# Kernel optimization log

Hardware: AMD Instinct MI355X
Metric: run time of the kernel (lower is better)

Reference implementation:

```python
import jax, jax.numpy as jnp
import numpy as np
import math

N, E, C, A, M, B, H = 50000, 600000, 32, 32, 32, 10, 64


def setup_inputs() -> dict:
    key = jax.random.key(0)
    ks = jax.random.split(key, 14)
    f = jnp.float32
    node_input = jax.random.normal(ks[0], (N, C), f)
    node_attr = jax.random.normal(ks[1], (N, A), f)
    node_deg = 1.0 + 31.0 * jax.random.uniform(ks[2], (N, 1), dtype=f)  # degrees >= 1
    edge_src = jax.random.randint(ks[3], (E,), 0, N, jnp.int32)
    edge_dst = jax.random.randint(ks[4], (E,), 0, N, jnp.int32)
    edge_attr = jax.random.normal(ks[5], (E, 9), f)  # SH up to lmax=2: 1+3+5
    edge_length_embedded = jax.random.uniform(ks[6], (E, B), dtype=f)
    w_lin_in = jax.random.normal(ks[7], (C, A, C), f)    # FCTP(Cx0e, Ax0e -> Cx0e)
    w_lin_mask = jax.random.normal(ks[8], (C, A, M), f)  # FCTP scalar block of linear_mask
    w_out0 = jax.random.normal(ks[9], (C, A, M), f)      # linear_output, l=0 block
    w_out1 = jax.random.normal(ks[10], (C, A, M), f)     # l=1 block
    w_out2 = jax.random.normal(ks[11], (C, A, M), f)     # l=2 block
    W0 = jax.random.normal(ks[12], (B, H), f)            # radial net (edge2weight)
    W1 = jax.random.normal(ks[13], (H, 3 * C), f)        # -> tensor_edge.weight_numel = 3C ('uvu', v=1)
    return dict(node_input=node_input, node_attr=node_attr, node_deg=node_deg,
                edge_src=edge_src, edge_dst=edge_dst, edge_attr=edge_attr,
                edge_length_embedded=edge_length_embedded,
                w_lin_in=w_lin_in, w_lin_mask=w_lin_mask,
                w_out0=w_out0, w_out1=w_out1, w_out2=w_out2, W0=W0, W1=W1,
                numb=100, n=8)


def reference(node_input, node_attr, node_deg, edge_src, edge_dst, edge_attr,
              edge_length_embedded, w_lin_in, w_lin_mask, w_out0, w_out1, w_out2,
              W0, W1, numb, n):
    # GraphConvolution.forward with irreps_in=Cx0e, irreps_node_attr=Ax0e,
    # irreps_edge_attr=1x0e+1x1o+1x2e (lmax=2), irreps_out=Mx0e+Mx1o+Mx2e.
    nN = node_input.shape[0]
    inv_ca = 1.0 / math.sqrt(C * A)

    def fctp_scalar(x, z, w):  # FullyConnectedTensorProduct with all-scalar in1/in2
        return jnp.einsum('nu,nv,uvk->nk', x, z, w) * inv_ca

    # linear_input, then node_deg normalization
    h0 = fctp_scalar(node_input, node_attr, w_lin_in)            # [N, C]
    deg_isqrt = 1.0 / jnp.sqrt(node_deg)                          # [N, 1]
    nf = h0 * deg_isqrt
    # linear_mask: only 0e outputs have tp paths (scalars x scalars); 1o/2e are zero
    mask_scalar = fctp_scalar(node_input, node_attr, w_lin_mask)  # [N, M]

    # edge2weight radial MLP (e3nn FullyConnectedNet style: /sqrt(fan_in), silu hidden)
    h = jax.nn.silu(edge_length_embedded @ W0 * (1.0 / math.sqrt(B)))
    ew = h @ W1 * (1.0 / math.sqrt(H))                            # [E, 3C]
    w0e, w1o, w2e = ew[:, :C], ew[:, C:2 * C], ew[:, 2 * C:]

    # tensor_edge: 'uvu' 0e(x)l->l paths: out[u,m] = w[u]*x_src[u]*Y_l[m]
    xs = nf[edge_src]                                             # gather [E, C]
    m0 = (w0e * xs) * edge_attr[:, :1]                            # [E, C]
    m1 = (w1o * xs)[:, :, None] * edge_attr[:, None, 1:4]         # [E, C, 3]
    m2 = (w2e * xs)[:, :, None] * edge_attr[:, None, 4:9]         # [E, C, 5]

    # scatter-reduce to destination nodes, then deg normalization
    a0 = jax.ops.segment_sum(m0, edge_dst, num_segments=nN) * deg_isqrt
    a1 = jax.ops.segment_sum(m1, edge_dst, num_segments=nN) * deg_isqrt[:, :, None]
    a2 = jax.ops.segment_sum(m2, edge_dst, num_segments=nN) * deg_isqrt[:, :, None]

    # linear_output: FCTP(mid, Ax0e -> out); scalar attr mixes multiplicities per l
    out0 = jnp.einsum('nu,nv,uvk->nk', a0, node_attr, w_out0) * inv_ca        # [N, M]
    out1 = jnp.einsum('num,nv,uvk->nkm', a1, node_attr, w_out1) * inv_ca      # [N, M, 3]
    out2 = jnp.einsum('num,nv,uvk->nkm', a2, node_attr, w_out2) * inv_ca      # [N, M, 5]

    # c_s * node_mask + c_x * node_output; output_mask is 1 on 0e, 0 on 1o/2e
    c_s, c_x = math.sin(math.pi / 8), math.cos(math.pi / 8)
    scal = c_s * mask_scalar + c_x * out0
    return jnp.concatenate([scal, out1.reshape(nN, 3 * M), out2.reshape(nN, 5 * M)], axis=1)
```

## Files before the change

### kernel.cpp

```cpp
#include <hip/hip_runtime.h>

#define NC 32
#define NA 32
#define NB 10
#define NH 64

typedef __attribute__((ext_vector_type(8))) short bf16x8;
typedef __attribute__((ext_vector_type(4))) float f32x4;

static __device__ __forceinline__ unsigned short f2bf(float f) {
  union { float f; unsigned u; } v; v.f = f;
  unsigned r = v.u + 0x7fffu + ((v.u >> 16) & 1u);
  return (unsigned short)(r >> 16);
}
static __device__ __forceinline__ float bf2f(unsigned short b) {
  union { unsigned u; float f; } v; v.u = ((unsigned)b) << 16;
  return v.f;
}

__global__ void k_prep(const float* __restrict__ nattr, const float* __restrict__ ndeg,
                       const float* __restrict__ w0, const float* __restrict__ w1,
                       const float* __restrict__ w2, const float* __restrict__ w3,
                       const float* __restrict__ w4, const float* __restrict__ W1g,
                       unsigned short* __restrict__ zb, float* __restrict__ dis,
                       unsigned short* __restrict__ wrp, unsigned short* __restrict__ w1p,
                       int N) {
  int i = blockIdx.x * 256 + threadIdx.x;
  int nz = N * NC;
  if (i < nz) { zb[i] = f2bf(nattr[i]); return; }
  i -= nz;
  if (i < N) { dis[i] = rsqrtf(ndeg[i]); return; }
  i -= N;
  if (i < 5 * 32768) {
    int T = i >> 15, r = i & 32767;
    int t = r >> 9, l = (r >> 3) & 63, b = r & 7;
    int j = t * 16 + (l & 15);
    int u = j >> 5, k = j & 31, v = 8 * (l >> 4) + b;
    const float* w = (T == 0) ? w0 : (T == 1) ? w1 : (T == 2) ? w2 : (T == 3) ? w3 : w4;
    wrp[T * 32768 + (t * 64 + l) * 8 + b] = f2bf(w[u * 1024 + v * 32 + k] * (1.0f / 32.0f));
    return;
  }
  i -= 5 * 32768;
  if (i < 6144) {
    int c = i / 3072, r2 = i % 3072;
    int t = r2 >> 9, l = (r2 >> 3) & 63, b = r2 & 7;
    int k = 32 * c + 8 * (l >> 4) + b, col = 16 * t + (l & 15);
    w1p[i] = f2bf(W1g[k * 96 + col] * 0.125f);
  }
}

__global__ __launch_bounds__(512) void k_fctp(
    const unsigned short* __restrict__ wrp, const unsigned short* __restrict__ zb,
    const float* __restrict__ xp, int nm, int xnstr, int xoff,
    float* __restrict__ outp, int onstr,
    const float* __restrict__ scalep,
    const float* __restrict__ addp, float selfc, float addc) {
  __shared__ float zw[16 * 1025];
  __shared__ float xl[16][5][32];
  int tid = threadIdx.x;
  int lane = tid & 63, wv = tid >> 6;
  int nbase = blockIdx.x << 4;

  for (int i = tid; i < 16 * nm * 32; i += 512) {
    int n = i / (nm * 32); int rem = i - n * (nm * 32); int m = rem >> 5, u = rem & 31;
    xl[n][m][u] = xp[(nbase + n) * xnstr + xoff + m * 32 + u];
  }

  bf16x8 af = *(const bf16x8*)(zb + (nbase + (lane & 15)) * 32 + 8 * (lane >> 4));
  f32x4 acc[8];
#pragma unroll
  for (int i2 = 0; i2 < 8; ++i2) {
    int t = wv * 8 + i2;
    bf16x8 bfr = *(const bf16x8*)(wrp + (t * 64 + lane) * 8);
    f32x4 z4 = {0.f, 0.f, 0.f, 0.f};
    acc[i2] = __builtin_amdgcn_mfma_f32_16x16x32_bf16(af, bfr, z4, 0, 0, 0);
  }
  int rb = 4 * (lane >> 4);
#pragma unroll
  for (int i2 = 0; i2 < 8; ++i2) {
    int col = (wv * 8 + i2) * 16 + (lane & 15);
#pragma unroll
    for (int r = 0; r < 4; ++r) zw[(rb + r) * 1025 + col] = acc[i2][r];
  }
  __syncthreads();

  int n = tid >> 5, k = tid & 31;
  float sc = scalep ? scalep[nbase + n] : 1.0f;
  const float* zr = &zw[n * 1025];
  for (int m = 0; m < nm; ++m) {
    float s = 0.f;
#pragma unroll
    for (int u = 0; u < 32; ++u) s = fmaf(xl[n][m][u], zr[u * 32 + k], s);
    s *= sc;
    if (addp) s = selfc * s + addc * addp[(nbase + n) * 32 + k];
    outp[(nbase + n) * onstr + k * nm + m] = s;
  }
}

__global__ void k_count(const int* __restrict__ dst, int* __restrict__ cnt, int E) {
  int i = blockIdx.x * 256 + threadIdx.x;
  if (i < E) atomicAdd(&cnt[dst[i]], 1);
}
__global__ __launch_bounds__(512) void k_scan1(const int* __restrict__ cnt, int* __restrict__ exl,
                                               int* __restrict__ bsum, int n) {
  __shared__ int s[512];
  int t = threadIdx.x;
  int i = blockIdx.x * 512 + t;
  int v = (i < n) ? cnt[i] : 0;
  s[t] = v;
  __syncthreads();
  for (int off = 1; off < 512; off <<= 1) {
    int add = (t >= off) ? s[t - off] : 0;
    __syncthreads();
    s[t] += add;
    __syncthreads();
  }
  if (i < n) exl[i] = s[t] - v;
  if (t == 511) bsum[blockIdx.x] = s[511];
}
__global__ void k_scan2(int* __restrict__ bsum, int nb) {
  __shared__ int s[128];
  int t = threadIdx.x;
  int v = (t < nb) ? bsum[t] : 0;
  s[t] = v;
  __syncthreads();
  for (int off = 1; off < 128; off <<= 1) {
    int add = (t >= off) ? s[t - off] : 0;
    __syncthreads();
    s[t] += add;
    __syncthreads();
  }
  if (t < nb) bsum[t] = s[t] - v;
}
__global__ void k_scan3(int* __restrict__ off, const int* __restrict__ bbase,
                        int* __restrict__ cur, int N, int E) {
  int i = blockIdx.x * 256 + threadIdx.x;
  if (i < N) {
    int o = off[i] + bbase[i >> 9];
    off[i] = o;
    cur[i] = o;
  } else if (i == N) {
    off[N] = E;
  }
}
__global__ void k_fill(const int* __restrict__ dst, int* __restrict__ cur,
                       int* __restrict__ pos, int E) {
  int i = blockIdx.x * 256 + threadIdx.x;
  if (i < E) {
    pos[i] = atomicAdd(&cur[dst[i]], 1);
  }
}

__global__ __launch_bounds__(256) void k_mlp(const float* __restrict__ el,
                                             const float* __restrict__ W0g,
                                             const unsigned short* __restrict__ w1p,
                                             const int* __restrict__ pos,
                                             const int* __restrict__ esrc,
                                             const float* __restrict__ eattr,
                                             unsigned short* __restrict__ ewP,
                                             int* __restrict__ esrcP,
                                             float* __restrict__ eattrP, int E) {
  __shared__ float w0s[NB * NH];
  __shared__ __align__(16) unsigned short tile[64 * 104];
  __shared__ int posl[64];
  int tid = threadIdx.x;
  int ebase = blockIdx.x * 64;
  for (int i = tid; i < NB * NH; i += 256) w0s[i] = W0g[i] * 0.31622776601683794f;
  if (tid < 64) posl[tid] = pos[ebase + tid];
  __syncthreads();

  for (int i = tid; i < 64 * 10; i += 256) {
    int le = i / 10, c = i - le * 10;
    int p = posl[le];
    int e = ebase + le;
    if (c == 0) esrcP[p] = esrc[e];
    else eattrP[(size_t)p * 9 + (c - 1)] = eattr[(size_t)e * 9 + (c - 1)];
  }

  int lane = tid & 63, wv = tid >> 6;
  int eloc0 = wv * 16;
  int erow = ebase + eloc0 + (lane & 15);
  float elr[NB];
#pragma unroll
  for (int b = 0; b < NB; ++b) elr[b] = el[erow * NB + b];
  int g8 = 8 * (lane >> 4);
  bf16x8 afr[2];
#pragma unroll
  for (int c = 0; c < 2; ++c) {
#pragma unroll
    for (int b = 0; b < 8; ++b) {
      int j = 32 * c + g8 + b;
      float p = 0.f;
#pragma unroll
      for (int q = 0; q < NB; ++q) p = fmaf(elr[q], w0s[q * NH + j], p);
      float h = p / (1.f + __expf(-p));
      afr[c][b] = (short)f2bf(h);
    }
  }
  f32x4 acc[6];
#pragma unroll
  for (int t = 0; t < 6; ++t) { f32x4 z4 = {0.f, 0.f, 0.f, 0.f}; acc[t] = z4; }
#pragma unroll
  for (int c = 0; c < 2; ++c) {
#pragma unroll
    for (int t = 0; t < 6; ++t) {
      bf16x8 bfr = *(const bf16x8*)(w1p + ((c * 6 + t) * 64 + lane) * 8);
      acc[t] = __builtin_amdgcn_mfma_f32_16x16x32_bf16(afr[c], bfr, acc[t], 0, 0, 0);
    }
  }
  int rb = 4 * (lane >> 4);
#pragma unroll
  for (int t = 0; t < 6; ++t) {
    int col = 16 * t + (lane & 15);
#pragma unroll
    for (int r = 0; r < 4; ++r) {
      tile[(eloc0 + rb + r) * 104 + col] = f2bf(acc[t][r]);
    }
  }
  __syncthreads();
  for (int ch = tid; ch < 64 * 12; ch += 256) {
    int le = ch / 12, seg = ch - le * 12;
    int p = posl[le];
    *(uint4*)(ewP + (size_t)p * 96 + seg * 8) =
        *(const uint4*)(&tile[le * 104 + seg * 8]);
  }
}

__global__ __launch_bounds__(256) void k_gather(
    const int* __restrict__ off, const int* __restrict__ esrcP,
    const float* __restrict__ eattrP, const unsigned short* __restrict__ ewP,
    const float* __restrict__ nf, const float* __restrict__ dis,
    float* __restrict__ a_all, int N) {
  int hw = (blockIdx.x * 256 + threadIdx.x) >> 5;
  int u = threadIdx.x & 31;
  if (hw >= N) return;
  int beg = off[hw], end = off[hw + 1];
  float a0 = 0, a1x = 0, a1y = 0, a1z = 0, b0 = 0, b1 = 0, b2 = 0, b3 = 0, b4 = 0;
  float xs_next = 0.f;
  if (beg < end) {
    int s0 = esrcP[beg];
    xs_next = nf[(size_t)s0 * 32 + u];
  }
  for (int p = beg; p < end; ++p) {
    float xs = xs_next;
    if (p + 1 < end) {
      int s2 = esrcP[p + 1];
      xs_next = nf[(size_t)s2 * 32 + u];
    }
    const unsigned short* ewr = ewP + (size_t)p * 96;
    float w0 = bf2f(ewr[u]), w1 = bf2f(ewr[32 + u]), w2 = bf2f(ewr[64 + u]);
    const float* ea = eattrP + (size_t)p * 9;
    float t0 = w0 * xs, t1 = w1 * xs, t2 = w2 * xs;
    a0  = fmaf(t0, ea[0], a0);
    a1x = fmaf(t1, ea[1], a1x);
    a1y = fmaf(t1, ea[2], a1y);
    a1z = fmaf(t1, ea[3], a1z);
    b0  = fmaf(t2, ea[4], b0);
    b1  = fmaf(t2, ea[5], b1);
    b2  = fmaf(t2, ea[6], b2);
    b3  = fmaf(t2, ea[7], b3);
    b4  = fmaf(t2, ea[8], b4);
  }
  float d = dis[hw];
  float* ar = a_all + (size_t)hw * 288;
  ar[0 * 32 + u] = a0 * d;
  ar[1 * 32 + u] = a1x * d;
  ar[2 * 32 + u] = a1y * d;
  ar[3 * 32 + u] = a1z * d;
  ar[4 * 32 + u] = b0 * d;
  ar[5 * 32 + u] = b1 * d;
  ar[6 * 32 + u] = b2 * d;
  ar[7 * 32 + u] = b3 * d;
  ar[8 * 32 + u] = b4 * d;
}

extern "C" void kernel_launch(void* const* d_in, const int* in_sizes, int n_in,
                              void* d_out, int out_size, void* d_ws, size_t ws_size,
                              hipStream_t stream) {
  const float* node_input = (const float*)d_in[0];
  const float* node_attr  = (const float*)d_in[1];
  const float* node_deg   = (const float*)d_in[2];
  const int*   edge_src   = (const int*)d_in[3];
  const int*   edge_dst   = (const int*)d_in[4];
  const float* edge_attr  = (const float*)d_in[5];
  const float* el_emb     = (const float*)d_in[6];
  const float* w_lin_in   = (const float*)d_in[7];
  const float* w_lin_mask = (const float*)d_in[8];
  const float* w_out0     = (const float*)d_in[9];
  const float* w_out1     = (const float*)d_in[10];
  const float* w_out2     = (const float*)d_in[11];
  const float* W0         = (const float*)d_in[12];
  const float* W1         = (const float*)d_in[13];
  int N = in_sizes[0] / 32;
  int E = in_sizes[3];
  float* out = (float*)d_out;

  char* p = (char*)d_ws;
  auto carve = [&](size_t bytes) { char* r = p; p += (bytes + 255) & ~(size_t)255; return r; };
  unsigned short* ew  = (unsigned short*)carve((size_t)E * 96 * 2);
  float* eattrP       = (float*)carve((size_t)E * 9 * 4);
  int* esrcP          = (int*)carve((size_t)E * 4);
  float* a_all        = (float*)carve((size_t)N * 288 * 4);
  float* nf           = (float*)carve((size_t)N * 32 * 4);
  float* maskb        = (float*)carve((size_t)N * 32 * 4);
  unsigned short* zb  = (unsigned short*)carve((size_t)N * 32 * 2);
  float* dis          = (float*)carve((size_t)N * 4);
  unsigned short* wrp = (unsigned short*)carve(5 * 32768 * 2);
  unsigned short* w1p = (unsigned short*)carve(6144 * 2);
  int* cnt            = (int*)carve((size_t)N * 4);
  int* off            = (int*)carve((size_t)(N + 1) * 4);
  int* cur            = (int*)carve((size_t)N * 4);
  int* pos            = (int*)carve((size_t)E * 4);
  int* bsum           = (int*)carve(1024);

  hipMemsetAsync(cnt, 0, (size_t)N * 4, stream);

  int tot = N * 32 + N + 5 * 32768 + 6144;
  k_prep<<<(tot + 255) / 256, 256, 0, stream>>>(node_attr, node_deg, w_lin_in, w_lin_mask,
                                                w_out0, w_out1, w_out2, W1, zb, dis, wrp, w1p, N);

  const float c_s = 0.3826834323650898f;
  const float c_x = 0.9238795325112867f;
  int nblk = N / 16;

  k_fctp<<<nblk, 512, 0, stream>>>(wrp + 0 * 32768, zb, node_input, 1, 32, 0, nf, 32,
                                   dis, nullptr, 0.f, 0.f);
  k_fctp<<<nblk, 512, 0, stream>>>(wrp + 1 * 32768, zb, node_input, 1, 32, 0, maskb, 32,
                                   nullptr, nullptr, 0.f, 0.f);

  k_count<<<(E + 255) / 256, 256, 0, stream>>>(edge_dst, cnt, E);
  int nb1 = (N + 511) / 512;
  k_scan1<<<nb1, 512, 0, stream>>>(cnt, off, bsum, N);
  k_scan2<<<1, 128, 0, stream>>>(bsum, nb1);
  k_scan3<<<(N + 1 + 255) / 256, 256, 0, stream>>>(off, bsum, cur, N, E);
  k_fill<<<(E + 255) / 256, 256, 0, stream>>>(edge_dst, cur, pos, E);

  k_mlp<<<E / 64, 256, 0, stream>>>(el_emb, W0, w1p, pos, edge_src, edge_attr,
                                    ew, esrcP, eattrP, E);
  k_gather<<<(N * 32 + 255) / 256, 256, 0, stream>>>(off, esrcP, eattrP, ew, nf,
                                                     dis, a_all, N);

  k_fctp<<<nblk, 512, 0, stream>>>(wrp + 2 * 32768, zb, a_all, 1, 288, 0, out + 0, 288,
                                   nullptr, maskb, c_x, c_s);
  k_fctp<<<nblk, 512, 0, stream>>>(wrp + 3 * 32768, zb, a_all, 3, 288, 32, out + 32, 288,
                                   nullptr, nullptr, 0.f, 0.f);
  k_fctp<<<nblk, 512, 0, stream>>>(wrp + 4 * 32768, zb, a_all, 5, 288, 128, out + 128, 288,
                                   nullptr, nullptr, 0.f, 0.f);
}
```

Before: 488.6 us.

## Fuse FCTP launches, pack per-edge records, and split gather across half-waves

Folds the degree-count atomics into the prep kernel. The two input FCTPs are merged into one kernel, and the three output FCTPs into another, each working on 8 nodes per block. The MLP now writes one 256-byte packed record per edge: bf16 weights, bf16 edge attributes and a 16-bit source index. This replaces three separate sorted arrays. The gather assigns one wave per node, with each half-wave taking alternate edges and a shuffle to reduce. The aim is fewer launches and fewer scattered memory streams. In exchange, edge attributes drop to bf16 precision, source indices are truncated to 16 bits (only valid for N below 65536), and half of each 16x16 MFMA tile is wasted.

```diff
diff --git a/kernel.cpp b/kernel.cpp
--- a/kernel.cpp
+++ b/kernel.cpp
@@ -1,9 +1,9 @@
 #include <hip/hip_runtime.h>
 
 #define NC 32
-#define NA 32
 #define NB 10
 #define NH 64
+#define REC 128
 
 typedef __attribute__((ext_vector_type(8))) short bf16x8;
 typedef __attribute__((ext_vector_type(4))) float f32x4;
@@ -22,9 +22,10 @@
                        const float* __restrict__ w0, const float* __restrict__ w1,
                        const float* __restrict__ w2, const float* __restrict__ w3,
                        const float* __restrict__ w4, const float* __restrict__ W1g,
+                       const int* __restrict__ edst, int* __restrict__ cnt,
                        unsigned short* __restrict__ zb, float* __restrict__ dis,
                        unsigned short* __restrict__ wrp, unsigned short* __restrict__ w1p,
-                       int N) {
+                       int N, int E) {
   int i = blockIdx.x * 256 + threadIdx.x;
   int nz = N * NC;
   if (i < nz) { zb[i] = f2bf(nattr[i]); return; }
@@ -46,61 +47,59 @@
     int t = r2 >> 9, l = (r2 >> 3) & 63, b = r2 & 7;
     int k = 32 * c + 8 * (l >> 4) + b, col = 16 * t + (l & 15);
     w1p[i] = f2bf(W1g[k * 96 + col] * 0.125f);
-  }
-}
-
-__global__ __launch_bounds__(512) void k_fctp(
+    return;
+  }
+  i -= 6144;
+  if (i < E) atomicAdd(&cnt[edst[i]], 1);
+}
+
+__global__ __launch_bounds__(256) void k_nfmask(
     const unsigned short* __restrict__ wrp, const unsigned short* __restrict__ zb,
-    const float* __restrict__ xp, int nm, int xnstr, int xoff,
-    float* __restrict__ outp, int onstr,
-    const float* __restrict__ scalep,
-    const float* __restrict__ addp, float selfc, float addc) {
-  __shared__ float zw[16 * 1025];
-  __shared__ float xl[16][5][32];
+    const float* __restrict__ x_in, const float* __restrict__ dis,
+    float* __restrict__ nf, float* __restrict__ maskb, int N) {
+  __shared__ float zw[8 * 1024];
+  __shared__ float xl[8][32];
   int tid = threadIdx.x;
   int lane = tid & 63, wv = tid >> 6;
-  int nbase = blockIdx.x << 4;
-
-  for (int i = tid; i < 16 * nm * 32; i += 512) {
-    int n = i / (nm * 32); int rem = i - n * (nm * 32); int m = rem >> 5, u = rem & 31;
-    xl[n][m][u] = xp[(nbase + n) * xnstr + xoff + m * 32 + u];
-  }
-
-  bf16x8 af = *(const bf16x8*)(zb + (nbase + (lane & 15)) * 32 + 8 * (lane >> 4));
-  f32x4 acc[8];
-#pragma unroll
-  for (int i2 = 0; i2 < 8; ++i2) {
-    int t = wv * 8 + i2;
-    bf16x8 bfr = *(const bf16x8*)(wrp + (t * 64 + lane) * 8);
-    f32x4 z4 = {0.f, 0.f, 0.f, 0.f};
-    acc[i2] = __builtin_amdgcn_mfma_f32_16x16x32_bf16(af, bfr, z4, 0, 0, 0);
-  }
+  int nbase = blockIdx.x << 3;
+
+  for (int i = tid; i < 8 * 32; i += 256) xl[i >> 5][i & 31] = x_in[nbase * 32 + i];
+
+  int arow = lane & 15;
+  bf16x8 af = {0,0,0,0,0,0,0,0};
+  if (arow < 8) af = *(const bf16x8*)(zb + (nbase + arow) * 32 + 8 * (lane >> 4));
+
   int rb = 4 * (lane >> 4);
-#pragma unroll
-  for (int i2 = 0; i2 < 8; ++i2) {
-    int col = (wv * 8 + i2) * 16 + (lane & 15);
-#pragma unroll
-    for (int r = 0; r < 4; ++r) zw[(rb + r) * 1025 + col] = acc[i2][r];
-  }
-  __syncthreads();
-
   int n = tid >> 5, k = tid & 31;
-  float sc = scalep ? scalep[nbase + n] : 1.0f;
-  const float* zr = &zw[n * 1025];
-  for (int m = 0; m < nm; ++m) {
+  for (int T = 0; T < 2; ++T) {
+    f32x4 acc[16];
+#pragma unroll
+    for (int i2 = 0; i2 < 16; ++i2) {
+      int t = wv * 16 + i2;
+      bf16x8 bfr = *(const bf16x8*)(wrp + ((size_t)T * 32768) + ((size_t)t * 64 + lane) * 8);
+      f32x4 z4 = {0.f, 0.f, 0.f, 0.f};
+      acc[i2] = __builtin_amdgcn_mfma_f32_16x16x32_bf16(af, bfr, z4, 0, 0, 0);
+    }
+    __syncthreads();
+    if (rb < 8) {
+#pragma unroll
+      for (int i2 = 0; i2 < 16; ++i2) {
+        int col = (wv * 16 + i2) * 16 + (lane & 15);
+#pragma unroll
+        for (int r = 0; r < 4; ++r) zw[(rb + r) * 1024 + col] = acc[i2][r];
+      }
+    }
+    __syncthreads();
     float s = 0.f;
-#pragma unroll
-    for (int u = 0; u < 32; ++u) s = fmaf(xl[n][m][u], zr[u * 32 + k], s);
-    s *= sc;
-    if (addp) s = selfc * s + addc * addp[(nbase + n) * 32 + k];
-    outp[(nbase + n) * onstr + k * nm + m] = s;
-  }
-}
-
-__global__ void k_count(const int* __restrict__ dst, int* __restrict__ cnt, int E) {
-  int i = blockIdx.x * 256 + threadIdx.x;
-  if (i < E) atomicAdd(&cnt[dst[i]], 1);
-}
+    const float* zr = &zw[n * 1024];
+#pragma unroll
+    for (int u = 0; u < 32; ++u) s = fmaf(xl[n][u], zr[u * 32 + k], s);
+    int gn = nbase + n;
+    if (T == 0) nf[gn * 32 + k] = s * dis[gn];
+    else        maskb[gn * 32 + k] = s;
+  }
+}
+
 __global__ __launch_bounds__(512) void k_scan1(const int* __restrict__ cnt, int* __restrict__ exl,
                                                int* __restrict__ bsum, int n) {
   __shared__ int s[512];
@@ -146,36 +145,32 @@
 __global__ void k_fill(const int* __restrict__ dst, int* __restrict__ cur,
                        int* __restrict__ pos, int E) {
   int i = blockIdx.x * 256 + threadIdx.x;
-  if (i < E) {
-    pos[i] = atomicAdd(&cur[dst[i]], 1);
-  }
-}
-
+  if (i < E) pos[i] = atomicAdd(&cur[dst[i]], 1);
+}
+
+#define TS 136
 __global__ __launch_bounds__(256) void k_mlp(const float* __restrict__ el,
                                              const float* __restrict__ W0g,
                                              const unsigned short* __restrict__ w1p,
                                              const int* __restrict__ pos,
                                              const int* __restrict__ esrc,
                                              const float* __restrict__ eattr,
-                                             unsigned short* __restrict__ ewP,
-                                             int* __restrict__ esrcP,
-                                             float* __restrict__ eattrP, int E) {
+                                             unsigned short* __restrict__ recs, int E) {
   __shared__ float w0s[NB * NH];
-  __shared__ __align__(16) unsigned short tile[64 * 104];
+  __shared__ __align__(16) unsigned short tile[64 * TS];
   __shared__ int posl[64];
   int tid = threadIdx.x;
   int ebase = blockIdx.x * 64;
   for (int i = tid; i < NB * NH; i += 256) w0s[i] = W0g[i] * 0.31622776601683794f;
   if (tid < 64) posl[tid] = pos[ebase + tid];
-  __syncthreads();
 
   for (int i = tid; i < 64 * 10; i += 256) {
     int le = i / 10, c = i - le * 10;
-    int p = posl[le];
     int e = ebase + le;
-    if (c == 0) esrcP[p] = esrc[e];
-    else eattrP[(size_t)p * 9 + (c - 1)] = eattr[(size_t)e * 9 + (c - 1)];
-  }
+    if (c < 9) tile[le * TS + 96 + c] = f2bf(eattr[(size_t)e * 9 + c]);
+    else       tile[le * TS + 105] = (unsigned short)esrc[e];
+  }
+  __syncthreads();
 
   int lane = tid & 63, wv = tid >> 6;
   int eloc0 = wv * 16;
@@ -213,65 +208,130 @@
   for (int t = 0; t < 6; ++t) {
     int col = 16 * t + (lane & 15);
 #pragma unroll
-    for (int r = 0; r < 4; ++r) {
-      tile[(eloc0 + rb + r) * 104 + col] = f2bf(acc[t][r]);
-    }
+    for (int r = 0; r < 4; ++r) tile[(eloc0 + rb + r) * TS + col] = f2bf(acc[t][r]);
   }
   __syncthreads();
-  for (int ch = tid; ch < 64 * 12; ch += 256) {
-    int le = ch / 12, seg = ch - le * 12;
-    int p = posl[le];
-    *(uint4*)(ewP + (size_t)p * 96 + seg * 8) =
-        *(const uint4*)(&tile[le * 104 + seg * 8]);
+  for (int ch = tid; ch < 64 * 16; ch += 256) {
+    int le = ch >> 4, seg = ch & 15;
+    size_t p = (size_t)posl[le];
+    *(uint4*)(recs + p * REC + seg * 8) = *(const uint4*)(&tile[le * TS + seg * 8]);
   }
 }
 
 __global__ __launch_bounds__(256) void k_gather(
-    const int* __restrict__ off, const int* __restrict__ esrcP,
-    const float* __restrict__ eattrP, const unsigned short* __restrict__ ewP,
+    const int* __restrict__ off, const unsigned short* __restrict__ recs,
     const float* __restrict__ nf, const float* __restrict__ dis,
     float* __restrict__ a_all, int N) {
-  int hw = (blockIdx.x * 256 + threadIdx.x) >> 5;
-  int u = threadIdx.x & 31;
+  int hw = blockIdx.x * 4 + (threadIdx.x >> 6);
+  int lane = threadIdx.x & 63;
+  int u = lane & 31, half = lane >> 5;
   if (hw >= N) return;
   int beg = off[hw], end = off[hw + 1];
   float a0 = 0, a1x = 0, a1y = 0, a1z = 0, b0 = 0, b1 = 0, b2 = 0, b3 = 0, b4 = 0;
   float xs_next = 0.f;
-  if (beg < end) {
-    int s0 = esrcP[beg];
+  int p0 = beg + half;
+  if (p0 < end) {
+    int s0 = recs[(size_t)p0 * REC + 105];
     xs_next = nf[(size_t)s0 * 32 + u];
   }
-  for (int p = beg; p < end; ++p) {
+  for (int p = p0; p < end; p += 2) {
     float xs = xs_next;
-    if (p + 1 < end) {
-      int s2 = esrcP[p + 1];
+    int p2 = p + 2;
+    if (p2 < end) {
+      int s2 = recs[(size_t)p2 * REC + 105];
       xs_next = nf[(size_t)s2 * 32 + u];
     }
-    const unsigned short* ewr = ewP + (size_t)p * 96;
-    float w0 = bf2f(ewr[u]), w1 = bf2f(ewr[32 + u]), w2 = bf2f(ewr[64 + u]);
-    const float* ea = eattrP + (size_t)p * 9;
+    const unsigned short* r = recs + (size_t)p * REC;
+    float w0 = bf2f(r[u]), w1 = bf2f(r[32 + u]), w2 = bf2f(r[64 + u]);
     float t0 = w0 * xs, t1 = w1 * xs, t2 = w2 * xs;
-    a0  = fmaf(t0, ea[0], a0);
-    a1x = fmaf(t1, ea[1], a1x);
-    a1y = fmaf(t1, ea[2], a1y);
-    a1z = fmaf(t1, ea[3], a1z);
-    b0  = fmaf(t2, ea[4], b0);
-    b1  = fmaf(t2, ea[5], b1);
-    b2  = fmaf(t2, ea[6], b2);
-    b3  = fmaf(t2, ea[7], b3);
-    b4  = fmaf(t2, ea[8], b4);
-  }
-  float d = dis[hw];
-  float* ar = a_all + (size_t)hw * 288;
-  ar[0 * 32 + u] = a0 * d;
-  ar[1 * 32 + u] = a1x * d;
-  ar[2 * 32 + u] = a1y * d;
-  ar[3 * 32 + u] = a1z * d;
-  ar[4 * 32 + u] = b0 * d;
-  ar[5 * 32 + u] = b1 * d;
-  ar[6 * 32 + u] = b2 * d;
-  ar[7 * 32 + u] = b3 * d;
-  ar[8 * 32 + u] = b4 * d;
+    a0  = fmaf(t0, bf2f(r[96]), a0);
+    a1x = fmaf(t1, bf2f(r[97]), a1x);
+    a1y = fmaf(t1, bf2f(r[98]), a1y);
+    a1z = fmaf(t1, bf2f(r[99]), a1z);
+    b0  = fmaf(t2, bf2f(r[100]), b0);
+    b1  = fmaf(t2, bf2f(r[101]), b1);
+    b2  = fmaf(t2, bf2f(r[102]), b2);
+    b3  = fmaf(t2, bf2f(r[103]), b3);
+    b4  = fmaf(t2, bf2f(r[104]), b4);
+  }
+  a0 += __shfl_xor(a0, 32, 64);  a1x += __shfl_xor(a1x, 32, 64);
+  a1y += __shfl_xor(a1y, 32, 64); a1z += __shfl_xor(a1z, 32, 64);
+  b0 += __shfl_xor(b0, 32, 64);  b1 += __shfl_xor(b1, 32, 64);
+  b2 += __shfl_xor(b2, 32, 64);  b3 += __shfl_xor(b3, 32, 64);
+  b4 += __shfl_xor(b4, 32, 64);
+  if (half == 0) {
+    float d = dis[hw];
+    float* ar = a_all + (size_t)hw * 288;
+    ar[0 * 32 + u] = a0 * d;
+    ar[1 * 32 + u] = a1x * d;
+    ar[2 * 32 + u] = a1y * d;
+    ar[3 * 32 + u] = a1z * d;
+    ar[4 * 32 + u] = b0 * d;
+    ar[5 * 32 + u] = b1 * d;
+    ar[6 * 32 + u] = b2 * d;
+    ar[7 * 32 + u] = b3 * d;
+    ar[8 * 32 + u] = b4 * d;
+  }
+}
+
+__global__ __launch_bounds__(256) void k_out(
+    const unsigned short* __restrict__ wrp, const unsigned short* __restrict__ zb,
+    const float* __restrict__ a_all, const float* __restrict__ maskb,
+    float* __restrict__ out, int N) {
+  __shared__ float zw[8 * 1024];
+  __shared__ float xl[8][9][32];
+  int tid = threadIdx.x;
+  int lane = tid & 63, wv = tid >> 6;
+  int nbase = blockIdx.x << 3;
+
+  for (int i = tid; i < 8 * 288; i += 256) {
+    int n2 = i / 288, rem = i - n2 * 288;
+    xl[n2][rem >> 5][rem & 31] = a_all[(size_t)(nbase + n2) * 288 + rem];
+  }
+
+  int arow = lane & 15;
+  bf16x8 af = {0,0,0,0,0,0,0,0};
+  if (arow < 8) af = *(const bf16x8*)(zb + (nbase + arow) * 32 + 8 * (lane >> 4));
+
+  const float c_s = 0.3826834323650898f;
+  const float c_x = 0.9238795325112867f;
+  int rb = 4 * (lane >> 4);
+  int n = tid >> 5, k = tid & 31;
+  const int nmT[3] = {1, 3, 5};
+  const int moff[3] = {0, 1, 4};
+  const int ooff[3] = {0, 32, 128};
+
+  for (int T = 0; T < 3; ++T) {
+    f32x4 acc[16];
+#pragma unroll
+    for (int i2 = 0; i2 < 16; ++i2) {
+      int t = wv * 16 + i2;
+      bf16x8 bfr = *(const bf16x8*)(wrp + ((size_t)(2 + T) * 32768) + ((size_t)t * 64 + lane) * 8);
+      f32x4 z4 = {0.f, 0.f, 0.f, 0.f};
+      acc[i2] = __builtin_amdgcn_mfma_f32_16x16x32_bf16(af, bfr, z4, 0, 0, 0);
+    }
+    __syncthreads();
+    if (rb < 8) {
+#pragma unroll
+      for (int i2 = 0; i2 < 16; ++i2) {
+        int col = (wv * 16 + i2) * 16 + (lane & 15);
+#pragma unroll
+        for (int r = 0; r < 4; ++r) zw[(rb + r) * 1024 + col] = acc[i2][r];
+      }
+    }
+    __syncthreads();
+    const float* zr = &zw[n * 1024];
+    int gn = nbase + n;
+    int nm = nmT[T];
+    for (int m = 0; m < nm; ++m) {
+      float s = 0.f;
+      const float* xr = xl[n][moff[T] + m];
+#pragma unroll
+      for (int u = 0; u < 32; ++u) s = fmaf(xr[u], zr[u * 32 + k], s);
+      if (T == 0) s = c_x * s + c_s * maskb[(size_t)gn * 32 + k];
+      out[(size_t)gn * 288 + ooff[T] + k * nm + m] = s;
+    }
+  }
 }
 
 extern "C" void kernel_launch(void* const* d_in, const int* in_sizes, int n_in,
@@ -297,9 +357,7 @@
 
   char* p = (char*)d_ws;
   auto carve = [&](size_t bytes) { char* r = p; p += (bytes + 255) & ~(size_t)255; return r; };
-  unsigned short* ew  = (unsigned short*)carve((size_t)E * 96 * 2);
-  float* eattrP       = (float*)carve((size_t)E * 9 * 4);
-  int* esrcP          = (int*)carve((size_t)E * 4);
+  unsigned short* recs = (unsigned short*)carve((size_t)E * REC * 2);
   float* a_all        = (float*)carve((size_t)N * 288 * 4);
   float* nf           = (float*)carve((size_t)N * 32 * 4);
   float* maskb        = (float*)carve((size_t)N * 32 * 4);
@@ -315,35 +373,21 @@
 
   hipMemsetAsync(cnt, 0, (size_t)N * 4, stream);
 
-  int tot = N * 32 + N + 5 * 32768 + 6144;
+  int tot = N * 32 + N + 5 * 32768 + 6144 + E;
   k_prep<<<(tot + 255) / 256, 256, 0, stream>>>(node_attr, node_deg, w_lin_in, w_lin_mask,
-                                                w_out0, w_out1, w_out2, W1, zb, dis, wrp, w1p, N);
-
-  const float c_s = 0.3826834323650898f;
-  const float c_x = 0.9238795325112867f;
-  int nblk = N / 16;
-
-  k_fctp<<<nblk, 512, 0, stream>>>(wrp + 0 * 32768, zb, node_input, 1, 32, 0, nf, 32,
-                                   dis, nullptr, 0.f, 0.f);
-  k_fctp<<<nblk, 512, 0, stream>>>(wrp + 1 * 32768, zb, node_input, 1, 32, 0, maskb, 32,
-                                   nullptr, nullptr, 0.f, 0.f);
-
-  k_count<<<(E + 255) / 256, 256, 0, stream>>>(edge_dst, cnt, E);
+                                                w_out0, w_out1, w_out2, W1, edge_dst, cnt,
+                                                zb, dis, wrp, w1p, N, E);
+
+  k_nfmask<<<N / 8, 256, 0, stream>>>(wrp, zb, node_input, dis, nf, maskb, N);
+
   int nb1 = (N + 511) / 512;
   k_scan1<<<nb1, 512, 0, stream>>>(cnt, off, bsum, N);
   k_scan2<<<1, 128, 0, stream>>>(bsum, nb1);
   k_scan3<<<(N + 1 + 255) / 256, 256, 0, stream>>>(off, bsum, cur, N, E);
   k_fill<<<(E + 255) / 256, 256, 0, stream>>>(edge_dst, cur, pos, E);
 
-  k_mlp<<<E / 64, 256, 0, stream>>>(el_emb, W0, w1p, pos, edge_src, edge_attr,
-                                    ew, esrcP, eattrP, E);
-  k_gather<<<(N * 32 + 255) / 256, 256, 0, stream>>>(off, esrcP, eattrP, ew, nf,
-                                                     dis, a_all, N);
-
-  k_fctp<<<nblk, 512, 0, stream>>>(wrp + 2 * 32768, zb, a_all, 1, 288, 0, out + 0, 288,
-                                   nullptr, maskb, c_x, c_s);
-  k_fctp<<<nblk, 512, 0, stream>>>(wrp + 3 * 32768, zb, a_all, 3, 288, 32, out + 32, 288,
-                                   nullptr, nullptr, 0.f, 0.f);
-  k_fctp<<<nblk, 512, 0, stream>>>(wrp + 4 * 32768, zb, a_all, 5, 288, 128, out + 128, 288,
-                                   nullptr, nullptr, 0.f, 0.f);
-}
+  k_mlp<<<E / 64, 256, 0, stream>>>(el_emb, W0, w1p, pos, edge_src, edge_attr, recs, E);
+  k_gather<<<(N + 3) / 4, 256, 0, stream>>>(off, recs, nf, dis, a_all, N);
+
+  k_out<<<N / 8, 256, 0, stream>>>(wrp, zb, a_all, maskb, out, N);
+}
```

Result: slower. 502.1 us (+2.8%).
